# Performance work log

Measured on AMD Instinct MI355X. Metric: run time of the kernel, lower is better.

Reference implementation:

```python
import jax, jax.numpy as jnp
import numpy as np
from jax import lax


def setup_inputs() -> dict:
    key = jax.random.key(0)
    ks = jax.random.split(key, 16)
    def rn(k, shape, s=0.05):
        return (jax.random.normal(k, shape) * s).astype(jnp.float32)
    B, N, F = 16, 1024, 200
    return dict(
        x=jax.random.normal(ks[0], (B, 1, N, F), dtype=jnp.float32),
        gat_W=rn(ks[1], (F, F)), att_src=rn(ks[2], (F,)), att_dst=rn(ks[3], (F,)), gat_b=rn(ks[4], (F,)),
        conv1_w=rn(ks[5], (40, 1, 1, 26)), conv1_b=rn(ks[6], (40,)),
        bn1_g=jnp.ones((40,), jnp.float32), bn1_b=jnp.zeros((40,), jnp.float32),
        bn1_m=jnp.zeros((40,), jnp.float32), bn1_v=jnp.ones((40,), jnp.float32),
        conv2_w=rn(ks[7], (40, 40, N), 0.01), conv2_b=rn(ks[8], (40,)),
        bn2_g=jnp.ones((40,), jnp.float32), bn2_b=jnp.zeros((40,), jnp.float32),
        bn2_m=jnp.zeros((40,), jnp.float32), bn2_v=jnp.ones((40,), jnp.float32),
        projc_w=rn(ks[9], (40, 40)), projc_b=rn(ks[10], (40,)),
        W1=rn(ks[11], (1400, 1024)), b1=rn(ks[12], (1024,)),
        W2=rn(ks[13], (1024, 1024)), b2=rn(ks[14], (1024,)),
        ln_g=jnp.ones((1024,), jnp.float32), ln_b=jnp.zeros((1024,), jnp.float32),
    )


def _bn(y, g, b, m, v, eps=1e-5):
    # eval-mode BatchNorm over channel axis 1
    shp = (1, -1) + (1,) * (y.ndim - 2)
    return (y - m.reshape(shp)) * (g.reshape(shp) / jnp.sqrt(v.reshape(shp) + eps)) + b.reshape(shp)


def reference(x, gat_W, att_src, att_dst, gat_b, conv1_w, conv1_b,
              bn1_g, bn1_b, bn1_m, bn1_v, conv2_w, conv2_b,
              bn2_g, bn2_b, bn2_m, bn2_v, projc_w, projc_b,
              W1, b1, W2, b2, ln_g, ln_b):
    B, _, N, F = x.shape  # (16,1,1024,200)
    # --- EEG_GAT (PyG GATConv, heads=1). edge_index only covers nodes 0..N-1;
    # add_self_loops applies to all B*N nodes -> first graph is dense attention
    # (complete graph incl. self), remaining nodes see only their self-loop.
    h = x.reshape(B * N, F) @ gat_W               # (B*N, 200)
    a_s = h[:N] @ att_src                          # source scores, first graph
    a_d = h[:N] @ att_dst                          # target scores
    logits = jax.nn.leaky_relu(a_s[None, :] + a_d[:, None], 0.2)  # [target i, source j]
    out0 = jax.nn.softmax(logits, axis=1) @ h[:N]  # (N, 200)
    gat = (jnp.concatenate([out0, h[N:]], axis=0) + gat_b).reshape(B, 1, N, F)
    x = x + gat  # ResidualAdd (dropout in eval = identity)
    # --- PatchEmbedding shallownet
    y = lax.conv_general_dilated(x, conv1_w, (1, 1), 'VALID',
                                 dimension_numbers=('NCHW', 'OIHW', 'NCHW'))
    y = y + conv1_b[None, :, None, None]           # (B,40,1024,175)
    y = y.reshape(B, 40, N, 35, 5).mean(-1)        # AvgPool2d (1,5) stride (1,5)
    y = jax.nn.elu(_bn(y, bn1_g, bn1_b, bn1_m, bn1_v))
    y = jnp.einsum('bchw,och->bow', y, conv2_w) + conv2_b[None, :, None]  # Conv2d(40,40,(1024,1)) -> (B,40,35)
    y = jax.nn.elu(_bn(y, bn2_g, bn2_b, bn2_m, bn2_v))
    # projection 1x1 conv then rearrange 'b e h w -> b (h w) e' then flatten
    y = jnp.einsum('bow,eo->bew', y, projc_w) + projc_b[None, :, None]
    y = y.transpose(0, 2, 1).reshape(B, -1)        # (B, 1400)
    # --- Proj_eeg
    z = y @ W1 + b1
    z = z + (jax.nn.gelu(z, approximate=False) @ W2 + b2)
    mu = z.mean(-1, keepdims=True)
    var = ((z - mu) ** 2).mean(-1, keepdims=True)
    return (z - mu) / jnp.sqrt(var + 1e-5) * ln_g + ln_b
```

## Files before the change

### kernel.cpp

```cpp
#include <hip/hip_runtime.h>
#include <math.h>

typedef __attribute__((ext_vector_type(8))) short short8;
typedef __attribute__((ext_vector_type(4))) float f32x4;

__device__ __forceinline__ unsigned f2bf(float f) {
  unsigned u = __float_as_uint(f);
  return (u + 0x7FFFu + ((u >> 16) & 1u)) >> 16;
}
__device__ __forceinline__ unsigned pk2(float lo, float hi) {
  return f2bf(lo) | (f2bf(hi) << 16);
}

#define WS_X1    0
#define WS_W2P   3328000
#define WS_AS    4966400
#define WS_AD    4967424
#define WS_WEFB  4968464
#define WS_S1    4969664
#define WS_SH1   4969704
#define WS_S2    4969744
#define WS_SH2   4969784
#define WS_H     4970496
#define WS_P     5232640
#define WS_HT    5494784
#define WS_Y3P   WS_P
#define WS_Y5    8400768
#define WS_ZP    8455936
#define WS_Z2P   8570624
#define WS_WPT   8701696
#define WS_Y2    8730368

__global__ __launch_bounds__(256) void k0_prep(const float* __restrict__ gat_W,
                        const float* __restrict__ conv1_w, const float* __restrict__ conv1_b,
                        const float* __restrict__ bn1_g, const float* __restrict__ bn1_b,
                        const float* __restrict__ bn1_m, const float* __restrict__ bn1_v,
                        const float* __restrict__ conv2_b,
                        const float* __restrict__ bn2_g, const float* __restrict__ bn2_b,
                        const float* __restrict__ bn2_m, const float* __restrict__ bn2_v,
                        const float* __restrict__ w2,
                        float* __restrict__ ws) {
  int bx = blockIdx.x, t = threadIdx.x;
  if (bx < 224) {
    unsigned short* wpt = (unsigned short*)(ws + WS_WPT);
    int idx = bx * 256 + t;
    int n = idx / 224, k = idx % 224;
    float v = (n < 200 && k < 200) ? gat_W[k * 200 + n] : 0.f;
    wpt[idx] = (unsigned short)f2bf(v);
    return;
  }
  if (bx == 224) {
    if (t < 48) {
      unsigned short* wb = (unsigned short*)(ws + WS_WEFB);
      float wv[30];
      if (t < 40) {
        for (int j = 0; j < 30; ++j) {
          float s = 0.f;
          for (int tt = 0; tt < 5; ++tt) {
            int k = j - tt;
            if (k >= 0 && k < 26) s += conv1_w[t * 26 + k];
          }
          wv[j] = s * 0.2f;
        }
      }
      for (int k = 0; k < 32; ++k)
        wb[t * 32 + k] = (unsigned short)f2bf((t < 40 && k < 30) ? wv[k] : 0.f);
    }
    if (t < 40) {
      float s1 = bn1_g[t] * rsqrtf(bn1_v[t] + 1e-5f);
      ws[WS_S1 + t] = s1;
      ws[WS_SH1 + t] = bn1_b[t] + (conv1_b[t] - bn1_m[t]) * s1;
      float s2 = bn2_g[t] * rsqrtf(bn2_v[t] + 1e-5f);
      ws[WS_S2 + t] = s2;
      ws[WS_SH2 + t] = bn2_b[t] + (conv2_b[t] - bn2_m[t]) * s2;
    }
    return;
  }
  __shared__ unsigned short lds[2560];
  int q = bx - 225;
  int c8 = q / 6, o0 = (q % 6) * 8;
  unsigned short* w2p = (unsigned short*)(ws + WS_W2P);
#pragma unroll
  for (int i = 0; i < 10; ++i) {
    int e = i * 256 + t;
    int o = e / 320, rr = e % 320;
    int c = rr / 8, nl = rr % 8;
    int oa = o0 + o;
    float v = (oa < 40) ? w2[(oa * 40 + c) * 1024 + c8 * 8 + nl] : 0.f;
    lds[o * 320 + nl * 40 + c] = (unsigned short)f2bf(v);
  }
  __syncthreads();
  uint4* src = (uint4*)lds;
  uint4* dst = (uint4*)(w2p + (c8 * 48 + o0) * 320);
  for (int i = t; i < 320; i += 256) dst[i] = src[i];
}

__global__ __launch_bounds__(256) void k1_mfma(const float* __restrict__ x,
                                               const unsigned short* __restrict__ wpt,
                                               const float* __restrict__ gat_b,
                                               float* __restrict__ h,
                                               unsigned short* __restrict__ hT,
                                               float* __restrict__ x1) {
  __shared__ unsigned short As[64 * 232];
  __shared__ unsigned short Bt[64 * 232];
  int t = threadIdx.x;
  int wave = t >> 6, lane = t & 63;
  int m16 = lane & 15, quad = lane >> 4;
  int row0 = blockIdx.x * 64;
  {
    int m = t >> 2, kq = (t & 3) * 8;
    const float* xr = x + (row0 + m) * 200;
#pragma unroll
    for (int s = 0; s < 7; ++s) {
      int kg = s * 32 + kq;
      uint4 pv;
      if (kg + 8 <= 200) {
        float4 a = *(const float4*)(xr + kg);
        float4 b = *(const float4*)(xr + kg + 4);
        pv.x = pk2(a.x, a.y); pv.y = pk2(a.z, a.w);
        pv.z = pk2(b.x, b.y); pv.w = pk2(b.z, b.w);
      } else {
        float e[8];
#pragma unroll
        for (int q = 0; q < 8; ++q) e[q] = (kg + q < 200) ? xr[kg + q] : 0.f;
        pv.x = pk2(e[0], e[1]); pv.y = pk2(e[2], e[3]);
        pv.z = pk2(e[4], e[5]); pv.w = pk2(e[6], e[7]);
      }
      *(uint4*)&As[m * 232 + kg] = pv;
    }
  }
  __syncthreads();
  for (int c = 0; c < 4; ++c) {
    int n0 = c * 64;
    for (int i = t; i < 1792; i += 256) {
      int row = i / 28, ch = i % 28;
      *(short8*)&Bt[row * 232 + ch * 8] = *(const short8*)&wpt[(n0 + row) * 224 + ch * 8];
    }
    __syncthreads();
    f32x4 acc[4];
#pragma unroll
    for (int nt = 0; nt < 4; ++nt) acc[nt] = (f32x4){0.f, 0.f, 0.f, 0.f};
#pragma unroll
    for (int s = 0; s < 7; ++s) {
      short8 af = *(const short8*)&As[(wave * 16 + m16) * 232 + s * 32 + quad * 8];
      int kb = s * 32 + quad * 8;
#pragma unroll
      for (int nt = 0; nt < 4; ++nt) {
        short8 bf = *(const short8*)&Bt[(nt * 16 + m16) * 232 + kb];
        acc[nt] = __builtin_amdgcn_mfma_f32_16x16x32_bf16(af, bf, acc[nt], 0, 0, 0);
      }
    }
    if (blockIdx.x < 16) {
#pragma unroll
      for (int nt = 0; nt < 4; ++nt) {
        int col = n0 + nt * 16 + m16;
#pragma unroll
        for (int r = 0; r < 4; ++r) {
          int row = row0 + wave * 16 + quad * 4 + r;
          float v = acc[nt][r];
          h[row * 256 + col] = v;
          hT[col * 1024 + row] = (unsigned short)f2bf(v);
        }
      }
    } else {
#pragma unroll
      for (int nt = 0; nt < 4; ++nt) {
        int col = n0 + nt * 16 + m16;
        if (col < 200) {
          float gb = gat_b[col];
#pragma unroll
          for (int r = 0; r < 4; ++r) {
            int row = row0 + wave * 16 + quad * 4 + r;
            x1[row * 200 + col] = x[row * 200 + col] + acc[nt][r] + gb;
          }
        }
      }
    }
    __syncthreads();
  }
}

__global__ __launch_bounds__(256) void k1b_scores(const float* __restrict__ h,
                                                  const float* __restrict__ att_src,
                                                  const float* __restrict__ att_dst,
                                                  float* __restrict__ as_,
                                                  float* __restrict__ ad_) {
  int t = threadIdx.x;
  int wave = t >> 6, lane = t & 63;
  int r = blockIdx.x * 4 + wave;
  float s = 0.f, d = 0.f;
  if (lane < 50) {
    float4 v = *(const float4*)(h + r * 256 + lane * 4);
    float4 a = *(const float4*)(att_src + lane * 4);
    float4 dd = *(const float4*)(att_dst + lane * 4);
    s = v.x * a.x + v.y * a.y + v.z * a.z + v.w * a.w;
    d = v.x * dd.x + v.y * dd.y + v.z * dd.z + v.w * dd.w;
  }
#pragma unroll
  for (int off = 32; off > 0; off >>= 1) {
    s += __shfl_down(s, off);
    d += __shfl_down(d, off);
  }
  if (lane == 0) {
    as_[r] = s;
    ad_[r] = d;
  }
}

__global__ __launch_bounds__(256) void kP(const float* __restrict__ as_,
                                          const float* __restrict__ ad_,
                                          unsigned short* __restrict__ Pb) {
  __shared__ float rb[256];
  int t = threadIdx.x, i = blockIdx.x;
  float a0 = as_[t], a1 = as_[256 + t], a2 = as_[512 + t], a3 = as_[768 + t];
  rb[t] = fmaxf(fmaxf(a0, a1), fmaxf(a2, a3));
  __syncthreads();
  for (int st = 128; st > 0; st >>= 1) {
    if (t < st) rb[t] = fmaxf(rb[t], rb[t + st]);
    __syncthreads();
  }
  float maxs = rb[0];
  __syncthreads();
  float ad = ad_[i];
  float mv = maxs + ad;
  float M = mv >= 0.f ? mv : 0.2f * mv;
  float av[4] = {a0, a1, a2, a3};
  float p[4];
  float s = 0.f;
#pragma unroll
  for (int q = 0; q < 4; ++q) {
    float v = av[q] + ad;
    float l = v >= 0.f ? v : 0.2f * v;
    p[q] = __expf(l - M);
    s += p[q];
  }
  rb[t] = s;
  __syncthreads();
  for (int st = 128; st > 0; st >>= 1) {
    if (t < st) rb[t] += rb[t + st];
    __syncthreads();
  }
  float inv = 1.f / rb[0];
#pragma unroll
  for (int q = 0; q < 4; ++q)
    Pb[i * 1024 + q * 256 + t] = (unsigned short)f2bf(p[q] * inv);
}

__global__ __launch_bounds__(256) void kAttn(const unsigned short* __restrict__ Pb,
                                             const unsigned short* __restrict__ hT,
                                             const float* __restrict__ x,
                                             const float* __restrict__ gat_b,
                                             float* __restrict__ x1) {
  __shared__ float red[4][1024];
  int t = threadIdx.x;
  int wave = t >> 6, lane = t & 63;
  int l15 = lane & 15, quad = lane >> 4;
  int i0 = blockIdx.x * 16, f0 = blockIdx.y * 64;
  int arow = i0 + l15;
  f32x4 acc[4];
#pragma unroll
  for (int nt = 0; nt < 4; ++nt) acc[nt] = (f32x4){0.f, 0.f, 0.f, 0.f};
#pragma unroll
  for (int ks = 0; ks < 8; ++ks) {
    int koff = wave * 256 + ks * 32 + quad * 8;
    short8 a = *(const short8*)&Pb[arow * 1024 + koff];
#pragma unroll
    for (int nt = 0; nt < 4; ++nt) {
      short8 bf = *(const short8*)&hT[(f0 + nt * 16 + l15) * 1024 + koff];
      acc[nt] = __builtin_amdgcn_mfma_f32_16x16x32_bf16(a, bf, acc[nt], 0, 0, 0);
    }
  }
#pragma unroll
  for (int nt = 0; nt < 4; ++nt)
#pragma unroll
    for (int r = 0; r < 4; ++r)
      red[wave][(quad * 4 + r) * 64 + nt * 16 + l15] = acc[nt][r];
  __syncthreads();
#pragma unroll
  for (int e = 0; e < 4; ++e) {
    int idx = t * 4 + e;
    int row = idx >> 6, col = idx & 63;
    int cg = f0 + col;
    if (cg < 200) {
      float s = red[0][idx] + red[1][idx] + red[2][idx] + red[3][idx];
      int rg = i0 + row;
      x1[rg * 200 + cg] = x[rg * 200 + cg] + s + gat_b[cg];
    }
  }
}

__global__ __launch_bounds__(256) void k3a_conv1(const float* __restrict__ x1,
                                                 const unsigned short* __restrict__ weffB,
                                                 const float* __restrict__ ws,
                                                 unsigned short* __restrict__ y2) {
  int t = threadIdx.x;
  int wave = t >> 6, lane = t & 63;
  int l15 = lane & 15, quad = lane >> 4;
  int tile = blockIdx.x * 4 + wave;
  int row = tile * 16 + l15;
  int nn = row / 35;
  int p = row - nn * 35;
  short8 bw[3];
#pragma unroll
  for (int nt = 0; nt < 3; ++nt)
    bw[nt] = *(const short8*)&weffB[(nt * 16 + l15) * 32 + quad * 8];
  const float* xr = x1 + nn * 200 + p * 5;
  int k0 = quad * 8;
  float e[8];
#pragma unroll
  for (int j = 0; j < 8; ++j) {
    int k = k0 + j;
    e[j] = (k < 30) ? xr[k] : 0.f;
  }
  short8 xf;
  ((uint*)&xf)[0] = pk2(e[0], e[1]);
  ((uint*)&xf)[1] = pk2(e[2], e[3]);
  ((uint*)&xf)[2] = pk2(e[4], e[5]);
  ((uint*)&xf)[3] = pk2(e[6], e[7]);
  unsigned short* yrow = y2 + row * 40;
#pragma unroll
  for (int nt = 0; nt < 3; ++nt) {
    f32x4 z = {0.f, 0.f, 0.f, 0.f};
    f32x4 c4 = __builtin_amdgcn_mfma_f32_16x16x32_bf16(bw[nt], xf, z, 0, 0, 0);
    int c0 = nt * 16 + quad * 4;
    if (c0 < 40) {
      float4 s1q = *(const float4*)(ws + WS_S1 + c0);
      float4 sh1q = *(const float4*)(ws + WS_SH1 + c0);
      float v0 = c4[0] * s1q.x + sh1q.x;
      float v1 = c4[1] * s1q.y + sh1q.y;
      float v2 = c4[2] * s1q.z + sh1q.z;
      float v3 = c4[3] * s1q.w + sh1q.w;
      v0 = v0 > 0.f ? v0 : __expf(v0) - 1.f;
      v1 = v1 > 0.f ? v1 : __expf(v1) - 1.f;
      v2 = v2 > 0.f ? v2 : __expf(v2) - 1.f;
      v3 = v3 > 0.f ? v3 : __expf(v3) - 1.f;
      uint2 pv;
      pv.x = pk2(v0, v1);
      pv.y = pk2(v2, v3);
      *(uint2*)&yrow[c0] = pv;
    }
  }
}

__global__ __launch_bounds__(256) void k3b_conv2(const unsigned short* __restrict__ y2,
                                                 const unsigned short* __restrict__ w2pre,
                                                 float* __restrict__ y3p) {
  __shared__ float red[2][48 * 49];
  int t = threadIdx.x;
  int wave = t >> 6, lane = t & 63;
  int l15 = lane & 15, quad = lane >> 4;
  int b = blockIdx.x, kc = blockIdx.y;
  const unsigned short* Ab = y2 + (b * 1024 + kc * 16) * 1400;
  int pA[3];
#pragma unroll
  for (int mt = 0; mt < 3; ++mt) {
    int p = mt * 16 + l15;
    pA[mt] = p > 34 ? 34 : p;
  }
  f32x4 acc[3][3];
#pragma unroll
  for (int mt = 0; mt < 3; ++mt)
#pragma unroll
    for (int nt = 0; nt < 3; ++nt) acc[mt][nt] = (f32x4){0.f, 0.f, 0.f, 0.f};
#pragma unroll
  for (int j = 0; j < 5; ++j) {
    int klocal = wave * 160 + j * 32 + quad * 8;
    int noff = klocal / 40;
    int c = klocal - noff * 40;
    const unsigned short* Ak = Ab + noff * 1400 + c;
    short8 a[3];
#pragma unroll
    for (int mt = 0; mt < 3; ++mt)
      a[mt] = *(const short8*)&Ak[pA[mt] * 40];
    int kg = kc * 640 + klocal;
    int slab = kg >> 8;
    slab = kg / 320;
    int kl = kg - slab * 320;
    const unsigned short* Bb = w2pre + slab * 48 * 320 + kl;
    short8 bb[3];
#pragma unroll
    for (int nt = 0; nt < 3; ++nt)
      bb[nt] = *(const short8*)&Bb[(nt * 16 + l15) * 320];
#pragma unroll
    for (int mt = 0; mt < 3; ++mt)
#pragma unroll
      for (int nt = 0; nt < 3; ++nt)
        acc[mt][nt] = __builtin_amdgcn_mfma_f32_16x16x32_bf16(a[mt], bb[nt], acc[mt][nt], 0, 0, 0);
  }
  if (wave < 2) {
    float* r = red[wave];
#pragma unroll
    for (int mt = 0; mt < 3; ++mt)
#pragma unroll
      for (int nt = 0; nt < 3; ++nt)
#pragma unroll
        for (int q = 0; q < 4; ++q)
          r[(mt * 16 + quad * 4 + q) * 49 + nt * 16 + l15] = acc[mt][nt][q];
  }
  __syncthreads();
  if (wave >= 2) {
    float* r = red[wave - 2];
#pragma unroll
    for (int mt = 0; mt < 3; ++mt)
#pragma unroll
      for (int nt = 0; nt < 3; ++nt)
#pragma unroll
        for (int q = 0; q < 4; ++q)
          r[(mt * 16 + quad * 4 + q) * 49 + nt * 16 + l15] += acc[mt][nt][q];
  }
  __syncthreads();
  float* dst = y3p + (b * 64 + kc) * 1400;
  for (int idx = t; idx < 1400; idx += 256) {
    int o = idx / 35, p = idx % 35;
    dst[idx] = red[0][p * 49 + o] + red[1][p * 49 + o];
  }
}

__global__ __launch_bounds__(256) void k4_fused(const float* __restrict__ y3p,
                                                const float* __restrict__ ws,
                                                const float* __restrict__ projc_w,
                                                const float* __restrict__ projc_b,
                                                float* __restrict__ y5) {
  __shared__ float tls[1400];
  int t = threadIdx.x, b = blockIdx.x;
  for (int idx = t; idx < 1400; idx += 256) {
    float s = 0.f;
#pragma unroll 4
    for (int q = 0; q < 64; ++q) s += y3p[(b * 64 + q) * 1400 + idx];
    int o = idx / 35;
    float v = s * ws[WS_S2 + o] + ws[WS_SH2 + o];
    tls[idx] = v > 0.f ? v : __expf(v) - 1.f;
  }
  __syncthreads();
  for (int idx = t; idx < 1400; idx += 256) {
    int p = idx / 40, e = idx % 40;
    float acc = projc_b[e];
    for (int o = 0; o < 40; ++o) acc += tls[o * 35 + p] * projc_w[e * 40 + o];
    y5[b * 1400 + idx] = acc;
  }
}

__global__ __launch_bounds__(256) void k5_fc1(const float* __restrict__ y5,
                                              const float* __restrict__ W1,
                                              float* __restrict__ zp) {
  __shared__ __align__(16) float yls[3200];
  int t = threadIdx.x;
  int nc = blockIdx.x, kc = blockIdx.y;
  for (int i = t; i < 800; i += 256) {
    int bb = i / 50, q = i % 50;
    ((float4*)yls)[bb * 50 + q] = *(const float4*)(y5 + bb * 1400 + kc * 200 + q * 4);
  }
  __syncthreads();
  int nl = t & 31, bg = t >> 5;
  int n = nc * 32 + nl;
  float acc0 = 0.f, acc1 = 0.f;
  const float* y0 = yls + (bg * 2) * 200;
  const float* y1 = yls + (bg * 2 + 1) * 200;
  for (int k = 0; k < 200; ++k) {
    float w = W1[(kc * 200 + k) * 1024 + n];
    acc0 += y0[k] * w;
    acc1 += y1[k] * w;
  }
  zp[(kc * 16 + bg * 2) * 1024 + n] = acc0;
  zp[(kc * 16 + bg * 2 + 1) * 1024 + n] = acc1;
}

__global__ __launch_bounds__(256) void k6_fc2(const float* __restrict__ zp,
                                              const float* __restrict__ b1,
                                              const float* __restrict__ W2,
                                              float* __restrict__ z2p) {
  __shared__ __align__(16) float gls[2048];
  int t = threadIdx.x;
  int nc = blockIdx.x, kc = blockIdx.y;
  for (int i = t; i < 2048; i += 256) {
    int bb = i >> 7, kk = i & 127;
    int np = kc * 128 + kk;
    float s = b1[np];
#pragma unroll
    for (int j = 0; j < 7; ++j) s += zp[(j * 16 + bb) * 1024 + np];
    gls[i] = 0.5f * s * (1.f + erff(s * 0.70710678f));
  }
  __syncthreads();
  int nl = t & 31, bg = t >> 5;
  int n = nc * 32 + nl;
  float acc0 = 0.f, acc1 = 0.f;
  const float* g0 = gls + (bg * 2) * 128;
  const float* g1 = gls + (bg * 2 + 1) * 128;
  for (int k = 0; k < 128; ++k) {
    float w = W2[(kc * 128 + k) * 1024 + n];
    acc0 += g0[k] * w;
    acc1 += g1[k] * w;
  }
  z2p[(kc * 16 + bg * 2) * 1024 + n] = acc0;
  z2p[(kc * 16 + bg * 2 + 1) * 1024 + n] = acc1;
}

__global__ __launch_bounds__(256) void k7_ln(const float* __restrict__ zp,
                                             const float* __restrict__ z2p,
                                             const float* __restrict__ b1,
                                             const float* __restrict__ b2,
                                             const float* __restrict__ ln_g,
                                             const float* __restrict__ ln_b,
                                             float* __restrict__ out) {
  __shared__ float r1[256], r2[256];
  int t = threadIdx.x, b = blockIdx.x;
  float4 v = *(const float4*)(b1 + t * 4);
  float4 bb2 = *(const float4*)(b2 + t * 4);
  v.x += bb2.x; v.y += bb2.y; v.z += bb2.z; v.w += bb2.w;
#pragma unroll
  for (int kc = 0; kc < 7; ++kc) {
    float4 p = *(const float4*)(zp + (kc * 16 + b) * 1024 + t * 4);
    v.x += p.x; v.y += p.y; v.z += p.z; v.w += p.w;
  }
#pragma unroll
  for (int kc = 0; kc < 8; ++kc) {
    float4 p = *(const float4*)(z2p + (kc * 16 + b) * 1024 + t * 4);
    v.x += p.x; v.y += p.y; v.z += p.z; v.w += p.w;
  }
  r1[t] = v.x + v.y + v.z + v.w;
  r2[t] = v.x * v.x + v.y * v.y + v.z * v.z + v.w * v.w;
  __syncthreads();
  for (int s = 128; s > 0; s >>= 1) {
    if (t < s) {
      r1[t] += r1[t + s];
      r2[t] += r2[t + s];
    }
    __syncthreads();
  }
  float mu = r1[0] * (1.f / 1024.f);
  float var = r2[0] * (1.f / 1024.f) - mu * mu;
  float rstd = rsqrtf(var + 1e-5f);
  float4 gg = *(const float4*)(ln_g + t * 4);
  float4 bb = *(const float4*)(ln_b + t * 4);
  float4 o;
  o.x = (v.x - mu) * rstd * gg.x + bb.x;
  o.y = (v.y - mu) * rstd * gg.y + bb.y;
  o.z = (v.z - mu) * rstd * gg.z + bb.z;
  o.w = (v.w - mu) * rstd * gg.w + bb.w;
  *(float4*)(out + b * 1024 + t * 4) = o;
}

extern "C" void kernel_launch(void* const* d_in, const int* in_sizes, int n_in,
                              void* d_out, int out_size, void* d_ws, size_t ws_size,
                              hipStream_t stream) {
  (void)in_sizes; (void)n_in; (void)out_size; (void)ws_size;
  const float* x       = (const float*)d_in[0];
  const float* gat_W   = (const float*)d_in[1];
  const float* att_src = (const float*)d_in[2];
  const float* att_dst = (const float*)d_in[3];
  const float* gat_b   = (const float*)d_in[4];
  const float* conv1_w = (const float*)d_in[5];
  const float* conv2_w = (const float*)d_in[11];
  const float* projc_w = (const float*)d_in[17];
  const float* projc_b = (const float*)d_in[18];
  const float* W1      = (const float*)d_in[19];
  const float* b1      = (const float*)d_in[20];
  const float* W2      = (const float*)d_in[21];
  const float* b2      = (const float*)d_in[22];
  const float* ln_g    = (const float*)d_in[23];
  const float* ln_b    = (const float*)d_in[24];
  float* ws  = (float*)d_ws;
  float* out = (float*)d_out;

  hipLaunchKernelGGL(k0_prep, dim3(993), dim3(256), 0, stream, gat_W, conv1_w,
                     (const float*)d_in[6], (const float*)d_in[7], (const float*)d_in[8],
                     (const float*)d_in[9], (const float*)d_in[10], (const float*)d_in[12],
                     (const float*)d_in[13], (const float*)d_in[14], (const float*)d_in[15],
                     (const float*)d_in[16], conv2_w, ws);
  hipLaunchKernelGGL(k1_mfma, dim3(256), dim3(256), 0, stream, x,
                     (const unsigned short*)(ws + WS_WPT), gat_b, ws + WS_H,
                     (unsigned short*)(ws + WS_HT), ws + WS_X1);
  hipLaunchKernelGGL(k1b_scores, dim3(256), dim3(256), 0, stream, ws + WS_H, att_src, att_dst,
                     ws + WS_AS, ws + WS_AD);
  hipLaunchKernelGGL(kP, dim3(1024), dim3(256), 0, stream, ws + WS_AS, ws + WS_AD,
                     (unsigned short*)(ws + WS_P));
  hipLaunchKernelGGL(kAttn, dim3(64, 4), dim3(256), 0, stream,
                     (const unsigned short*)(ws + WS_P),
                     (const unsigned short*)(ws + WS_HT), x, gat_b, ws + WS_X1);
  hipLaunchKernelGGL(k3a_conv1, dim3(8960), dim3(256), 0, stream, ws + WS_X1,
                     (const unsigned short*)(ws + WS_WEFB), ws,
                     (unsigned short*)(ws + WS_Y2));
  hipLaunchKernelGGL(k3b_conv2, dim3(16, 64), dim3(256), 0, stream,
                     (const unsigned short*)(ws + WS_Y2),
                     (const unsigned short*)(ws + WS_W2P), ws + WS_Y3P);
  hipLaunchKernelGGL(k4_fused, dim3(16), dim3(256), 0, stream, ws + WS_Y3P, ws, projc_w,
                     projc_b, ws + WS_Y5);
  hipLaunchKernelGGL(k5_fc1, dim3(32, 7), dim3(256), 0, stream, ws + WS_Y5, W1, ws + WS_ZP);
  hipLaunchKernelGGL(k6_fc2, dim3(32, 8), dim3(256), 0, stream, ws + WS_ZP, b1, W2,
                     ws + WS_Z2P);
  hipLaunchKernelGGL(k7_ln, dim3(16), dim3(256), 0, stream, ws + WS_ZP, ws + WS_Z2P, b1, b2,
                     ln_g, ln_b, out);
}
```

Measured before the change: 252.1 us.

## Fuse GAT score and softmax kernels into projection and attention kernels

Result: slower. 259.3 us (+2.9%).

```diff
diff --git a/kernel.cpp b/kernel.cpp
--- a/kernel.cpp
+++ b/kernel.cpp
@@ -97,12 +97,14 @@
 
 __global__ __launch_bounds__(256) void k1_mfma(const float* __restrict__ x,
                                                const unsigned short* __restrict__ wpt,
+                                               const float* __restrict__ att_src,
+                                               const float* __restrict__ att_dst,
                                                const float* __restrict__ gat_b,
-                                               float* __restrict__ h,
                                                unsigned short* __restrict__ hT,
-                                               float* __restrict__ x1) {
+                                               float* __restrict__ x1,
+                                               float* __restrict__ as_,
+                                               float* __restrict__ ad_) {
   __shared__ unsigned short As[64 * 232];
-  __shared__ unsigned short Bt[64 * 232];
   int t = threadIdx.x;
   int wave = t >> 6, lane = t & 63;
   int m16 = lane & 15, quad = lane >> 4;
@@ -130,13 +132,11 @@
     }
   }
   __syncthreads();
+  bool first = blockIdx.x < 16;
+  float sreg[4] = {0.f, 0.f, 0.f, 0.f};
+  float dreg[4] = {0.f, 0.f, 0.f, 0.f};
   for (int c = 0; c < 4; ++c) {
     int n0 = c * 64;
-    for (int i = t; i < 1792; i += 256) {
-      int row = i / 28, ch = i % 28;
-      *(short8*)&Bt[row * 232 + ch * 8] = *(const short8*)&wpt[(n0 + row) * 224 + ch * 8];
-    }
-    __syncthreads();
     f32x4 acc[4];
 #pragma unroll
     for (int nt = 0; nt < 4; ++nt) acc[nt] = (f32x4){0.f, 0.f, 0.f, 0.f};
@@ -146,20 +146,23 @@
       int kb = s * 32 + quad * 8;
 #pragma unroll
       for (int nt = 0; nt < 4; ++nt) {
-        short8 bf = *(const short8*)&Bt[(nt * 16 + m16) * 232 + kb];
+        short8 bf = *(const short8*)&wpt[(n0 + nt * 16 + m16) * 224 + kb];
         acc[nt] = __builtin_amdgcn_mfma_f32_16x16x32_bf16(af, bf, acc[nt], 0, 0, 0);
       }
     }
-    if (blockIdx.x < 16) {
+    if (first) {
 #pragma unroll
       for (int nt = 0; nt < 4; ++nt) {
         int col = n0 + nt * 16 + m16;
+        float sa = (col < 200) ? att_src[col] : 0.f;
+        float da = (col < 200) ? att_dst[col] : 0.f;
 #pragma unroll
         for (int r = 0; r < 4; ++r) {
           int row = row0 + wave * 16 + quad * 4 + r;
           float v = acc[nt][r];
-          h[row * 256 + col] = v;
           hT[col * 1024 + row] = (unsigned short)f2bf(v);
+          sreg[r] += v * sa;
+          dreg[r] += v * da;
         }
       }
     } else {
@@ -176,98 +179,89 @@
         }
       }
     }
-    __syncthreads();
-  }
-}
-
-__global__ __launch_bounds__(256) void k1b_scores(const float* __restrict__ h,
-                                                  const float* __restrict__ att_src,
-                                                  const float* __restrict__ att_dst,
-                                                  float* __restrict__ as_,
-                                                  float* __restrict__ ad_) {
-  int t = threadIdx.x;
-  int wave = t >> 6, lane = t & 63;
-  int r = blockIdx.x * 4 + wave;
-  float s = 0.f, d = 0.f;
-  if (lane < 50) {
-    float4 v = *(const float4*)(h + r * 256 + lane * 4);
-    float4 a = *(const float4*)(att_src + lane * 4);
-    float4 dd = *(const float4*)(att_dst + lane * 4);
-    s = v.x * a.x + v.y * a.y + v.z * a.z + v.w * a.w;
-    d = v.x * dd.x + v.y * dd.y + v.z * dd.z + v.w * dd.w;
-  }
-#pragma unroll
-  for (int off = 32; off > 0; off >>= 1) {
-    s += __shfl_down(s, off);
-    d += __shfl_down(d, off);
-  }
-  if (lane == 0) {
-    as_[r] = s;
-    ad_[r] = d;
-  }
-}
-
-__global__ __launch_bounds__(256) void kP(const float* __restrict__ as_,
-                                          const float* __restrict__ ad_,
-                                          unsigned short* __restrict__ Pb) {
-  __shared__ float rb[256];
-  int t = threadIdx.x, i = blockIdx.x;
-  float a0 = as_[t], a1 = as_[256 + t], a2 = as_[512 + t], a3 = as_[768 + t];
-  rb[t] = fmaxf(fmaxf(a0, a1), fmaxf(a2, a3));
-  __syncthreads();
-  for (int st = 128; st > 0; st >>= 1) {
-    if (t < st) rb[t] = fmaxf(rb[t], rb[t + st]);
-    __syncthreads();
-  }
-  float maxs = rb[0];
-  __syncthreads();
-  float ad = ad_[i];
-  float mv = maxs + ad;
-  float M = mv >= 0.f ? mv : 0.2f * mv;
-  float av[4] = {a0, a1, a2, a3};
-  float p[4];
-  float s = 0.f;
-#pragma unroll
-  for (int q = 0; q < 4; ++q) {
-    float v = av[q] + ad;
-    float l = v >= 0.f ? v : 0.2f * v;
-    p[q] = __expf(l - M);
-    s += p[q];
-  }
-  rb[t] = s;
-  __syncthreads();
-  for (int st = 128; st > 0; st >>= 1) {
-    if (t < st) rb[t] += rb[t + st];
-    __syncthreads();
-  }
-  float inv = 1.f / rb[0];
-#pragma unroll
-  for (int q = 0; q < 4; ++q)
-    Pb[i * 1024 + q * 256 + t] = (unsigned short)f2bf(p[q] * inv);
-}
-
-__global__ __launch_bounds__(256) void kAttn(const unsigned short* __restrict__ Pb,
+  }
+  if (first) {
+#pragma unroll
+    for (int r = 0; r < 4; ++r) {
+#pragma unroll
+      for (int off = 1; off < 16; off <<= 1) {
+        sreg[r] += __shfl_xor(sreg[r], off);
+        dreg[r] += __shfl_xor(dreg[r], off);
+      }
+    }
+    if (m16 == 0) {
+#pragma unroll
+      for (int r = 0; r < 4; ++r) {
+        int row = row0 + wave * 16 + quad * 4 + r;
+        as_[row] = sreg[r];
+        ad_[row] = dreg[r];
+      }
+    }
+  }
+}
+
+__global__ __launch_bounds__(256) void kAttn(const float* __restrict__ as_,
+                                             const float* __restrict__ ad_,
                                              const unsigned short* __restrict__ hT,
                                              const float* __restrict__ x,
                                              const float* __restrict__ gat_b,
                                              float* __restrict__ x1) {
+  __shared__ float asl[1024];
+  __shared__ float rs[256];
+  __shared__ float invl[16];
   __shared__ float red[4][1024];
   int t = threadIdx.x;
   int wave = t >> 6, lane = t & 63;
   int l15 = lane & 15, quad = lane >> 4;
   int i0 = blockIdx.x * 16, f0 = blockIdx.y * 64;
-  int arow = i0 + l15;
+  float4 av = ((const float4*)as_)[t];
+  ((float4*)asl)[t] = av;
+  float m0 = fmaxf(fmaxf(av.x, av.y), fmaxf(av.z, av.w));
+#pragma unroll
+  for (int off = 32; off > 0; off >>= 1) m0 = fmaxf(m0, __shfl_xor(m0, off));
+  if (lane == 0) rs[wave] = m0;
+  __syncthreads();
+  float maxs = fmaxf(fmaxf(rs[0], rs[1]), fmaxf(rs[2], rs[3]));
+  __syncthreads();
+  float ad = ad_[i0 + l15];
+  float mv = maxs + ad;
+  float M = mv >= 0.f ? mv : 0.2f * mv;
+  short8 af[8];
+  float psum = 0.f;
+#pragma unroll
+  for (int ks = 0; ks < 8; ++ks) {
+    int j0 = wave * 256 + ks * 32 + quad * 8;
+    float p[8];
+#pragma unroll
+    for (int m = 0; m < 8; ++m) {
+      float v = asl[j0 + m] + ad;
+      float l = v >= 0.f ? v : 0.2f * v;
+      p[m] = __expf(l - M);
+      psum += p[m];
+    }
+    ((uint*)&af[ks])[0] = pk2(p[0], p[1]);
+    ((uint*)&af[ks])[1] = pk2(p[2], p[3]);
+    ((uint*)&af[ks])[2] = pk2(p[4], p[5]);
+    ((uint*)&af[ks])[3] = pk2(p[6], p[7]);
+  }
+  rs[t] = psum;
+  __syncthreads();
+  if (t < 16) {
+    float s = 0.f;
+#pragma unroll
+    for (int g = 0; g < 16; ++g) s += rs[g * 16 + t];
+    invl[t] = 1.f / s;
+  }
   f32x4 acc[4];
 #pragma unroll
   for (int nt = 0; nt < 4; ++nt) acc[nt] = (f32x4){0.f, 0.f, 0.f, 0.f};
 #pragma unroll
   for (int ks = 0; ks < 8; ++ks) {
     int koff = wave * 256 + ks * 32 + quad * 8;
-    short8 a = *(const short8*)&Pb[arow * 1024 + koff];
 #pragma unroll
     for (int nt = 0; nt < 4; ++nt) {
       short8 bf = *(const short8*)&hT[(f0 + nt * 16 + l15) * 1024 + koff];
-      acc[nt] = __builtin_amdgcn_mfma_f32_16x16x32_bf16(a, bf, acc[nt], 0, 0, 0);
+      acc[nt] = __builtin_amdgcn_mfma_f32_16x16x32_bf16(af[ks], bf, acc[nt], 0, 0, 0);
     }
   }
 #pragma unroll
@@ -282,7 +276,7 @@
     int row = idx >> 6, col = idx & 63;
     int cg = f0 + col;
     if (cg < 200) {
-      float s = red[0][idx] + red[1][idx] + red[2][idx] + red[3][idx];
+      float s = (red[0][idx] + red[1][idx] + red[2][idx] + red[3][idx]) * invl[row];
       int rg = i0 + row;
       x1[rg * 200 + cg] = x[rg * 200 + cg] + s + gat_b[cg];
     }
@@ -373,8 +367,7 @@
     for (int mt = 0; mt < 3; ++mt)
       a[mt] = *(const short8*)&Ak[pA[mt] * 40];
     int kg = kc * 640 + klocal;
-    int slab = kg >> 8;
-    slab = kg / 320;
+    int slab = kg / 320;
     int kl = kg - slab * 320;
     const unsigned short* Bb = w2pre + slab * 48 * 320 + kl;
     short8 bb[3];
@@ -568,14 +561,9 @@
                      (const float*)d_in[13], (const float*)d_in[14], (const float*)d_in[15],
                      (const float*)d_in[16], conv2_w, ws);
   hipLaunchKernelGGL(k1_mfma, dim3(256), dim3(256), 0, stream, x,
-                     (const unsigned short*)(ws + WS_WPT), gat_b, ws + WS_H,
-                     (unsigned short*)(ws + WS_HT), ws + WS_X1);
-  hipLaunchKernelGGL(k1b_scores, dim3(256), dim3(256), 0, stream, ws + WS_H, att_src, att_dst,
-                     ws + WS_AS, ws + WS_AD);
-  hipLaunchKernelGGL(kP, dim3(1024), dim3(256), 0, stream, ws + WS_AS, ws + WS_AD,
-                     (unsigned short*)(ws + WS_P));
-  hipLaunchKernelGGL(kAttn, dim3(64, 4), dim3(256), 0, stream,
-                     (const unsigned short*)(ws + WS_P),
+                     (const unsigned short*)(ws + WS_WPT), att_src, att_dst, gat_b,
+                     (unsigned short*)(ws + WS_HT), ws + WS_X1, ws + WS_AS, ws + WS_AD);
+  hipLaunchKernelGGL(kAttn, dim3(64, 4), dim3(256), 0, stream, ws + WS_AS, ws + WS_AD,
                      (const unsigned short*)(ws + WS_HT), x, gat_b, ws + WS_X1);
   hipLaunchKernelGGL(k3a_conv1, dim3(8960), dim3(256), 0, stream, ws + WS_X1,
                      (const unsigned short*)(ws + WS_WEFB), ws,
```
